# Kernel tuning notes

Measured on AMD Instinct MI355X. Metric: run time of the kernel, lower is better.

The kernel has to match this reference:

```python
import jax, jax.numpy as jnp
import numpy as np

B, S, H, NH = 32, 512, 768, 12
EC, EU = 4, 4
CAP = 1.0
DH = H // NH
CAPACITY = int(CAP * B / EC)  # Switch-style capacity per common expert


def setup_inputs() -> dict:
    key = jax.random.key(0)
    ks = jax.random.split(key, 10)
    s = 0.02
    E = EC + EU  # experts stacked: [0:EC]=common, [EC:]=unique
    return {
        "hidden_states": jax.random.normal(ks[0], (B, S, H), jnp.float32),
        "attention_mask": jnp.zeros((B, S), jnp.float32),  # additive mask
        "Wq": jax.random.normal(ks[1], (E, H, H), jnp.float32) * s,
        "bq": jnp.zeros((E, H), jnp.float32),
        "Wk": jax.random.normal(ks[2], (E, H, H), jnp.float32) * s,
        "bk": jnp.zeros((E, H), jnp.float32),
        "Wv": jax.random.normal(ks[3], (E, H, H), jnp.float32) * s,
        "bv": jnp.zeros((E, H), jnp.float32),
        "Wo": jax.random.normal(ks[4], (E, H, H), jnp.float32) * s,
        "bo": jnp.zeros((E, H), jnp.float32),
        "Wsc": jax.random.normal(ks[5], (H, EC), jnp.float32) * s,
        "bsc": jnp.zeros((EC,), jnp.float32),
        "Wsu": jax.random.normal(ks[6], (H, EU), jnp.float32) * s,
        "bsu": jnp.zeros((EU,), jnp.float32),
    }


def reference(hidden_states, attention_mask, Wq, bq, Wk, bk, Wv, bv, Wo, bo,
              Wsc, bsc, Wsu, bsu):
    # ---- common routing (per-sequence top-1 over mean-pooled tokens) ----
    h_mean = hidden_states.mean(axis=1)                       # [B,H]
    pc = jax.nn.softmax(h_mean @ Wsc + bsc, axis=-1)          # [B,EC]
    rc = jnp.argmax(pc, axis=-1)                              # [B]
    pc_max = jnp.max(pc, axis=-1)                             # [B]
    # capacity drop: within each expert keep the CAPACITY highest-prob seqs
    order = jnp.argsort(-pc_max)                              # global desc sort
    oh = jax.nn.one_hot(rc[order], EC, dtype=jnp.int32)       # [B,EC]
    rank = jnp.take_along_axis(jnp.cumsum(oh, axis=0), rc[order][:, None], 1)[:, 0]
    kept = jnp.zeros((B,), bool).at[order].set(rank <= CAPACITY)

    # ---- unique routing for dropped sequences (mean is per-sequence, so
    #      computing on the full batch and masking matches torch) ----
    pu = jax.nn.softmax(h_mean @ Wsu + bsu, axis=-1)          # [B,EU]
    ru = jnp.argmax(pu, axis=-1)
    pu_max = jnp.max(pu, axis=-1)

    # per-sequence expert index into stacked [EC+EU] expert params
    eidx = jnp.where(kept, rc, EC + ru)                       # [B]
    # scaling factor p/stop_grad(p): ==1 in fwd, routes grads to the gate
    scale = jnp.where(kept,
                      pc_max / jax.lax.stop_gradient(pc_max),
                      pu_max / jax.lax.stop_gradient(pu_max))

    # ---- gather-dispatch: per-sequence expert weights ----
    Wq_b, Wk_b, Wv_b, Wo_b = Wq[eidx], Wk[eidx], Wv[eidx], Wo[eidx]  # [B,H,H]
    bq_b, bk_b, bv_b, bo_b = bq[eidx], bk[eidx], bv[eidx], bo[eidx]  # [B,H]

    def heads(t):  # [B,S,H] -> [B,NH,S,DH]
        return t.reshape(B, S, NH, DH).transpose(0, 2, 1, 3)

    q = heads(jnp.einsum('bsh,bhd->bsd', hidden_states, Wq_b) + bq_b[:, None, :])
    k = heads(jnp.einsum('bsh,bhd->bsd', hidden_states, Wk_b) + bk_b[:, None, :])
    v = heads(jnp.einsum('bsh,bhd->bsd', hidden_states, Wv_b) + bv_b[:, None, :])

    scores = jnp.einsum('bhsd,bhtd->bhst', q, k) / np.float32(np.sqrt(DH))
    scores = scores + attention_mask[:, None, None, :]        # additive mask
    attn = jax.nn.softmax(scores, axis=-1)
    ctx = jnp.einsum('bhst,bhtd->bhsd', attn, v)
    ctx = ctx.transpose(0, 2, 1, 3).reshape(B, S, H)

    out = jnp.einsum('bsh,bhd->bsd', ctx, Wo_b) + bo_b[:, None, :]
    return out * scale[:, None, None]
```

## Files before the change

### kernel.cpp

```cpp
#include <hip/hip_runtime.h>
#include <hip/hip_bf16.h>

#define B_ 32
#define S_ 512
#define H_ 768
#define NH_ 12
#define DH_ 64
#define EC_ 4
#define CAPN_ 8

using short8  = __attribute__((ext_vector_type(8))) short;
using floatx4 = __attribute__((ext_vector_type(4))) float;
using uint2v  = __attribute__((ext_vector_type(2))) unsigned;
using bf16 = __hip_bfloat16;

#define VMCNT(n) asm volatile("s_waitcnt vmcnt(" #n ")" ::: "memory")

__device__ __forceinline__ void gl_lds16(const void* g, void* l) {
  __builtin_amdgcn_global_load_lds(
      (const __attribute__((address_space(1))) unsigned int*)g,
      (__attribute__((address_space(3))) unsigned int*)l, 16, 0, 0);
}

__device__ __forceinline__ unsigned pk2(float lo, float hi) {
  __hip_bfloat162 h = __float22bfloat162_rn(make_float2(lo, hi));
  unsigned r;
  __builtin_memcpy(&r, &h, 4);
  return r;
}

__global__ void k_mean_convert(const float* __restrict__ X, bf16* __restrict__ Xh,
                               float* __restrict__ partial) {
  int idx = blockIdx.x * 256 + threadIdx.x;
  int b = idx / H_, h = idx - b * H_;
  int s0 = blockIdx.y * 64;
  size_t base = ((size_t)b * S_ + s0) * H_ + h;
  float sum = 0.f;
#pragma unroll 8
  for (int s = 0; s < 64; ++s) {
    float v = X[base + (size_t)s * H_];
    Xh[base + (size_t)s * H_] = __float2bfloat16(v);
    sum += v;
  }
  partial[(size_t)blockIdx.y * (B_ * H_) + idx] = sum;
}

__global__ void k_mean_reduce(const float* __restrict__ partial, float* __restrict__ hmean) {
  int idx = blockIdx.x * 256 + threadIdx.x;
  float s = 0.f;
#pragma unroll
  for (int c = 0; c < 8; ++c) s += partial[(size_t)c * (B_ * H_) + idx];
  hmean[idx] = s * (1.f / 512.f);
}

__global__ void k_wt(const float* __restrict__ Wq, const float* __restrict__ Wk,
                     const float* __restrict__ Wv, const float* __restrict__ Wo,
                     bf16* __restrict__ Wt) {
  __shared__ float tile[32][33];
  int z = blockIdx.z;
  const float* Wbase = (z < 8 ? Wq : z < 16 ? Wk : z < 24 ? Wv : Wo) + (size_t)(z & 7) * H_ * H_;
  int k0 = blockIdx.x * 32, n0 = blockIdx.y * 32;
  int tj = threadIdx.x & 31, ti = threadIdx.x >> 5;
#pragma unroll
  for (int r = 0; r < 4; ++r)
    tile[ti + r * 8][tj] = Wbase[(size_t)(k0 + ti + r * 8) * H_ + n0 + tj];
  __syncthreads();
  bf16* out = Wt + (size_t)z * H_ * H_;
#pragma unroll
  for (int r = 0; r < 4; ++r)
    out[(size_t)(n0 + ti + r * 8) * H_ + k0 + tj] = __float2bfloat16(tile[tj][ti + r * 8]);
}

__global__ void k_gate(const float* __restrict__ hmean,
                       const float* __restrict__ Wsc, const float* __restrict__ bsc,
                       const float* __restrict__ Wsu, const float* __restrict__ bsu,
                       float* __restrict__ logits) {
  int b = blockIdx.x;
  int t = threadIdx.x;
  int g = t >> 3, p = t & 7;
  const float* hm = hmean + (size_t)b * H_;
  const float* w;
  float bias;
  if (g < 4) { w = Wsc + g; bias = bsc[g]; }
  else       { w = Wsu + (g - 4); bias = bsu[g - 4]; }
  float acc = 0.f;
  for (int j = p; j < H_; j += 8) acc += hm[j] * w[j * 4];
  acc += __shfl_xor(acc, 1);
  acc += __shfl_xor(acc, 2);
  acc += __shfl_xor(acc, 4);
  if (p == 0) logits[b * 8 + g] = acc + bias;
}

__global__ void k_route2(const float* __restrict__ logits, int* __restrict__ eidx) {
  __shared__ float pcmax[B_];
  __shared__ int rc_s[B_], ru_s[B_];
  int t = threadIdx.x;
  if (t < B_) {
    float lg[8];
#pragma unroll
    for (int e = 0; e < 8; ++e) lg[e] = logits[t * 8 + e];
    float m = lg[0]; int a = 0;
    for (int e = 1; e < 4; ++e) if (lg[e] > m) { m = lg[e]; a = e; }
    float s = 0.f;
    for (int e = 0; e < 4; ++e) s += expf(lg[e] - m);
    pcmax[t] = 1.f / s;
    rc_s[t] = a;
    float mu = lg[4]; int au = 0;
    for (int e = 1; e < 4; ++e) if (lg[4 + e] > mu) { mu = lg[4 + e]; au = e; }
    ru_s[t] = au;
  }
  __syncthreads();
  if (t == 0) {
    bool used[B_], kept[B_];
    int cnt[EC_] = {0, 0, 0, 0};
    for (int i = 0; i < B_; ++i) used[i] = false;
    for (int i = 0; i < B_; ++i) {
      int best = 0; float bv = -1e30f;
      for (int j = 0; j < B_; ++j)
        if (!used[j] && pcmax[j] > bv) { bv = pcmax[j]; best = j; }
      used[best] = true;
      kept[best] = (++cnt[rc_s[best]] <= CAPN_);
    }
    for (int i = 0; i < B_; ++i)
      eidx[i] = kept[i] ? rc_s[i] : EC_ + ru_s[i];
  }
}

template <int OMODE, int NM>
__global__ __launch_bounds__(256, 3) void k_gemm(
    const bf16* __restrict__ A, const bf16* __restrict__ Wt,
    const float* __restrict__ bias0, const float* __restrict__ bias1,
    const float* __restrict__ bias2,
    void* out0, void* out1, void* out2,
    const int* __restrict__ eidx, int mat0) {
  __shared__ __align__(16) char lds[3][16384];
  const int nwg = 96 * NM * 8;
  int wg = blockIdx.x;
  int f = (wg & 7) * (nwg >> 3) + (wg >> 3);
  int b = f / (24 * NM);
  int r0 = f - b * 24 * NM;
  int mat = r0 / 24;
  int tile = r0 - mat * 24;
  int m0 = (tile & 3) * 128, n0 = (tile >> 2) * 128;
  int e = eidx[b];
  const bf16* Ab = A + (size_t)b * S_ * H_;
  const bf16* Wb = Wt + (size_t)((mat0 + mat) * 8 + e) * H_ * H_;
  const float* bias = ((mat == 0) ? bias0 : (mat == 1) ? bias1 : bias2) + (size_t)e * H_;
  void* outp = (mat == 0) ? out0 : (mat == 1) ? out1 : out2;

  int t = threadIdx.x, lane = t & 63, w = t >> 6;
  int wm = (w & 1) * 64, wn = (w >> 1) * 64;
  int lm = lane & 15, lq = lane >> 4;

  auto stage = [&](char* buf, int kt) {
#pragma unroll
    for (int r = 0; r < 4; ++r) {
      int c = t + r * 256;
      int isB = c >> 9;
      int cc = c & 511;
      int row = cc >> 2, pos = cc & 3;
      int kc = pos ^ (row & 3);
      const bf16* g = (isB ? Wb + (size_t)(n0 + row) * H_
                           : Ab + (size_t)(m0 + row) * H_) + kt * 32 + kc * 8;
      gl_lds16(g, buf + (size_t)c * 16);
    }
  };

  floatx4 acc[4][4] = {};
  stage(lds[0], 0);
  stage(lds[1], 1);
  VMCNT(4);
  __builtin_amdgcn_s_barrier();
  __builtin_amdgcn_sched_barrier(0);

  int cb = 0;
  for (int kt = 0; kt < 24; ++kt) {
    if (kt < 22) {
      int pb = cb + 2; if (pb >= 3) pb -= 3;
      stage(lds[pb], kt + 2);
    }
    const char* cur = lds[cb];
    short8 af[4], bfr[4];
#pragma unroll
    for (int mf = 0; mf < 4; ++mf) {
      int mm = wm + mf * 16 + lm;
      af[mf] = *(const short8*)(cur + mm * 64 + ((lq ^ (mm & 3)) * 16));
    }
#pragma unroll
    for (int nf = 0; nf < 4; ++nf) {
      int nn = wn + nf * 16 + lm;
      bfr[nf] = *(const short8*)(cur + 8192 + nn * 64 + ((lq ^ (nn & 3)) * 16));
    }
#pragma unroll
    for (int mf = 0; mf < 4; ++mf)
#pragma unroll
      for (int nf = 0; nf < 4; ++nf)
        acc[mf][nf] = __builtin_amdgcn_mfma_f32_16x16x32_bf16(af[mf], bfr[nf], acc[mf][nf], 0, 0, 0);
    if (kt < 23) {
      if (kt < 22) { VMCNT(4); } else { VMCNT(0); }
      __builtin_amdgcn_s_barrier();
      __builtin_amdgcn_sched_barrier(0);
    }
    ++cb; if (cb == 3) cb = 0;
  }

#pragma unroll
  for (int mf = 0; mf < 4; ++mf) {
#pragma unroll
    for (int nf = 0; nf < 4; ++nf) {
      int n = n0 + wn + nf * 16 + lm;
      float bv = bias[n];
      int mrow = m0 + wm + mf * 16 + lq * 4;
      size_t rowbase = ((size_t)b * S_ + mrow) * H_ + n;
#pragma unroll
      for (int r = 0; r < 4; ++r) {
        float v = acc[mf][nf][r] + bv;
        if (OMODE == 0) {
          if (mat == 2) {
            int s = mrow + r;
            ((bf16*)outp)[((size_t)(b * NH_ + (n >> 6))) * 32768 +
                          (size_t)(s >> 3) * 512 + (n & 63) * 8 + (s & 7)] =
                __float2bfloat16(v);
          } else {
            ((bf16*)outp)[rowbase + (size_t)r * H_] = __float2bfloat16(v);
          }
        } else {
          ((float*)outp)[rowbase + (size_t)r * H_] = v;
        }
      }
    }
  }
}

__global__ __launch_bounds__(256, 3) void k_attn(
    const bf16* __restrict__ Q, const bf16* __restrict__ K,
    const bf16* __restrict__ Vt, const float* __restrict__ mask,
    bf16* __restrict__ Ctx) {
  int bh = blockIdx.x;
  int b = bh / NH_, h = bh - b * NH_;
  int t = threadIdx.x, lane = t & 63, w = t >> 6;
  int lm = lane & 15, lq = lane >> 4;
  int q0 = blockIdx.y * 128 + w * 32;

  short8 qf[2][2];
#pragma unroll
  for (int mf = 0; mf < 2; ++mf)
#pragma unroll
    for (int kf = 0; kf < 2; ++kf)
      qf[mf][kf] = *(const short8*)(Q + ((size_t)(b * S_ + q0 + mf * 16 + lm)) * H_ +
                                    h * DH_ + kf * 32 + lq * 8);

  int kr = ((lm >> 2) << 3) + (lm & 3);
  const int koff[4] = {0, 4, 32, 36};
  const bf16* kbase = K + ((size_t)(b * S_) + kr) * H_ + h * DH_ + lq * 8;
  const bf16* vtb = Vt + ((size_t)(b * NH_ + h)) * 32768;
  const float* mbase = mask + (size_t)b * S_ + lq * 8;

  floatx4 oacc[2][4] = {};
  float m_[2] = {-1e30f, -1e30f}, l_[2] = {0.f, 0.f};

  for (int kt = 0; kt < 8; ++kt) {
    floatx4 sT[2][4] = {};
#pragma unroll
    for (int kf = 0; kf < 2; ++kf) {
      short8 kb4[4];
#pragma unroll
      for (int nf = 0; nf < 4; ++nf)
        kb4[nf] = *(const short8*)(kbase + (size_t)(kt * 64 + koff[nf]) * H_ + kf * 32);
#pragma unroll
      for (int mf = 0; mf < 2; ++mf)
#pragma unroll
        for (int nf = 0; nf < 4; ++nf)
          sT[mf][nf] = __builtin_amdgcn_mfma_f32_16x16x32_bf16(kb4[nf], qf[mf][kf], sT[mf][nf], 0, 0, 0);
    }
    short8 vf[2][4];
#pragma unroll
    for (int kf = 0; kf < 2; ++kf)
#pragma unroll
      for (int nf = 0; nf < 4; ++nf)
        vf[kf][nf] = *(const short8*)(vtb + (size_t)(kt * 8 + kf * 4 + lq) * 512 +
                                      (nf * 16 + lm) * 8);
    const floatx4* mp = (const floatx4*)(mbase + kt * 64);
    floatx4 mv[4] = {mp[0], mp[1], mp[8], mp[9]};

    short8 pf[2][2];
#pragma unroll
    for (int mf = 0; mf < 2; ++mf) {
      float p[4][4];
#pragma unroll
      for (int nf = 0; nf < 4; ++nf)
#pragma unroll
        for (int r = 0; r < 4; ++r)
          p[nf][r] = sT[mf][nf][r] * 0.125f + mv[nf][r];
      float t01 = fmaxf(fmaxf(fmaxf(p[0][0], p[0][1]), fmaxf(p[0][2], p[0][3])),
                        fmaxf(fmaxf(p[1][0], p[1][1]), fmaxf(p[1][2], p[1][3])));
      float t23 = fmaxf(fmaxf(fmaxf(p[2][0], p[2][1]), fmaxf(p[2][2], p[2][3])),
                        fmaxf(fmaxf(p[3][0], p[3][1]), fmaxf(p[3][2], p[3][3])));
      float tm = fmaxf(t01, t23);
      tm = fmaxf(tm, __shfl_xor(tm, 16));
      tm = fmaxf(tm, __shfl_xor(tm, 32));
      float mn = fmaxf(m_[mf], tm);
      float a = __expf(m_[mf] - mn);
      m_[mf] = mn;
      float ps = 0.f;
#pragma unroll
      for (int nf = 0; nf < 4; ++nf)
#pragma unroll
        for (int r = 0; r < 4; ++r) {
          p[nf][r] = __expf(p[nf][r] - mn);
          ps += p[nf][r];
        }
      ps += __shfl_xor(ps, 16);
      ps += __shfl_xor(ps, 32);
      l_[mf] = l_[mf] * a + ps;
#pragma unroll
      for (int nf = 0; nf < 4; ++nf) oacc[mf][nf] *= a;
      union { short8 s8; unsigned u[4]; } pku;
      pku.u[0] = pk2(p[0][0], p[0][1]); pku.u[1] = pk2(p[0][2], p[0][3]);
      pku.u[2] = pk2(p[1][0], p[1][1]); pku.u[3] = pk2(p[1][2], p[1][3]);
      pf[mf][0] = pku.s8;
      pku.u[0] = pk2(p[2][0], p[2][1]); pku.u[1] = pk2(p[2][2], p[2][3]);
      pku.u[2] = pk2(p[3][0], p[3][1]); pku.u[3] = pk2(p[3][2], p[3][3]);
      pf[mf][1] = pku.s8;
    }
#pragma unroll
    for (int kf = 0; kf < 2; ++kf)
#pragma unroll
      for (int mf = 0; mf < 2; ++mf)
#pragma unroll
        for (int nf = 0; nf < 4; ++nf)
          oacc[mf][nf] = __builtin_amdgcn_mfma_f32_16x16x32_bf16(vf[kf][nf], pf[mf][kf], oacc[mf][nf], 0, 0, 0);
  }
#pragma unroll
  for (int mf = 0; mf < 2; ++mf) {
    float inv = 1.f / l_[mf];
    bf16* op = Ctx + ((size_t)(b * S_ + q0 + mf * 16 + lm)) * H_ + h * DH_ + lq * 4;
#pragma unroll
    for (int nf = 0; nf < 4; ++nf) {
      uint2v o;
      o.x = pk2(oacc[mf][nf][0] * inv, oacc[mf][nf][1] * inv);
      o.y = pk2(oacc[mf][nf][2] * inv, oacc[mf][nf][3] * inv);
      *(uint2v*)(op + nf * 16) = o;
    }
  }
}

extern "C" void kernel_launch(void* const* d_in, const int* in_sizes, int n_in,
                              void* d_out, int out_size, void* d_ws, size_t ws_size,
                              hipStream_t stream) {
  const float* X    = (const float*)d_in[0];
  const float* mask = (const float*)d_in[1];
  const float* Wq   = (const float*)d_in[2];
  const float* bq   = (const float*)d_in[3];
  const float* Wk   = (const float*)d_in[4];
  const float* bk   = (const float*)d_in[5];
  const float* Wv   = (const float*)d_in[6];
  const float* bv   = (const float*)d_in[7];
  const float* Wo   = (const float*)d_in[8];
  const float* bo   = (const float*)d_in[9];
  const float* Wsc  = (const float*)d_in[10];
  const float* bsc  = (const float*)d_in[11];
  const float* Wsu  = (const float*)d_in[12];
  const float* bsu  = (const float*)d_in[13];

  char* ws = (char*)d_ws;
  int*   eidx    = (int*)ws;
  float* logits  = (float*)(ws + 128);
  float* partial = (float*)(ws + 1280);
  float* hmean   = (float*)(ws + 787712);
  bf16*  Xh      = (bf16*)(ws + 886016);
  bf16*  Wt      = (bf16*)(ws + 26051840);
  bf16*  qb      = (bf16*)(ws + 63800576);
  bf16*  kb      = (bf16*)(ws + 88966400);
  bf16*  Vt      = (bf16*)(ws + 114132224);
  bf16*  ctx     = Xh;

  k_mean_convert<<<dim3(96, 8), 256, 0, stream>>>(X, Xh, partial);
  k_mean_reduce<<<96, 256, 0, stream>>>(partial, hmean);
  k_wt<<<dim3(24, 24, 32), 256, 0, stream>>>(Wq, Wk, Wv, Wo, Wt);
  k_gate<<<B_, 64, 0, stream>>>(hmean, Wsc, bsc, Wsu, bsu, logits);
  k_route2<<<1, 64, 0, stream>>>(logits, eidx);
  k_gemm<0, 3><<<dim3(2304), 256, 0, stream>>>(Xh, Wt, bq, bk, bv,
                                               (void*)qb, (void*)kb, (void*)Vt, eidx, 0);
  k_attn<<<dim3(B_ * NH_, 4), 256, 0, stream>>>(qb, kb, Vt, mask, ctx);
  k_gemm<1, 1><<<dim3(768), 256, 0, stream>>>(ctx, Wt, bo, bo, bo,
                                              d_out, d_out, d_out, eidx, 3);
}
```

Baseline: 454.2 us.

## Merge prep kernels, fuse routing into one block, widen GEMM K-step to 64

Folds the mean/convert and weight-transpose kernels into a single launch, and merges the mean reduce, gate and routing into one 1024-thread block that keeps the per-sequence mean in LDS. The projection GEMM now stages 64-wide K slices with an 8-way XOR swizzle, double-buffering A and triple-buffering B, and halves the loop trip count. This raises LDS use to 80KB per block, so the launch bound drops to 2 blocks per CU. The intent is fewer launches and fewer barriers per K step, at the cost of occupancy and a serial single-block routing stage.

```diff
diff --git a/kernel.cpp b/kernel.cpp
--- a/kernel.cpp
+++ b/kernel.cpp
@@ -29,76 +29,81 @@
   return r;
 }
 
-__global__ void k_mean_convert(const float* __restrict__ X, bf16* __restrict__ Xh,
-                               float* __restrict__ partial) {
-  int idx = blockIdx.x * 256 + threadIdx.x;
-  int b = idx / H_, h = idx - b * H_;
-  int s0 = blockIdx.y * 64;
-  size_t base = ((size_t)b * S_ + s0) * H_ + h;
-  float sum = 0.f;
+__global__ void k_prep(const float* __restrict__ X, bf16* __restrict__ Xh,
+                       float* __restrict__ partial,
+                       const float* __restrict__ Wq, const float* __restrict__ Wk,
+                       const float* __restrict__ Wv, const float* __restrict__ Wo,
+                       bf16* __restrict__ Wt) {
+  __shared__ float tile[32][33];
+  int f = blockIdx.x;
+  if (f < 768) {
+    int bx = f % 96, by = f / 96;
+    int idx = bx * 256 + threadIdx.x;
+    int b = idx / H_, h = idx - b * H_;
+    int s0 = by * 64;
+    size_t base = ((size_t)b * S_ + s0) * H_ + h;
+    float sum = 0.f;
 #pragma unroll 8
-  for (int s = 0; s < 64; ++s) {
-    float v = X[base + (size_t)s * H_];
-    Xh[base + (size_t)s * H_] = __float2bfloat16(v);
-    sum += v;
-  }
-  partial[(size_t)blockIdx.y * (B_ * H_) + idx] = sum;
-}
-
-__global__ void k_mean_reduce(const float* __restrict__ partial, float* __restrict__ hmean) {
-  int idx = blockIdx.x * 256 + threadIdx.x;
-  float s = 0.f;
-#pragma unroll
-  for (int c = 0; c < 8; ++c) s += partial[(size_t)c * (B_ * H_) + idx];
-  hmean[idx] = s * (1.f / 512.f);
-}
-
-__global__ void k_wt(const float* __restrict__ Wq, const float* __restrict__ Wk,
-                     const float* __restrict__ Wv, const float* __restrict__ Wo,
-                     bf16* __restrict__ Wt) {
-  __shared__ float tile[32][33];
-  int z = blockIdx.z;
-  const float* Wbase = (z < 8 ? Wq : z < 16 ? Wk : z < 24 ? Wv : Wo) + (size_t)(z & 7) * H_ * H_;
-  int k0 = blockIdx.x * 32, n0 = blockIdx.y * 32;
-  int tj = threadIdx.x & 31, ti = threadIdx.x >> 5;
-#pragma unroll
-  for (int r = 0; r < 4; ++r)
-    tile[ti + r * 8][tj] = Wbase[(size_t)(k0 + ti + r * 8) * H_ + n0 + tj];
-  __syncthreads();
-  bf16* out = Wt + (size_t)z * H_ * H_;
-#pragma unroll
-  for (int r = 0; r < 4; ++r)
-    out[(size_t)(n0 + ti + r * 8) * H_ + k0 + tj] = __float2bfloat16(tile[tj][ti + r * 8]);
-}
-
-__global__ void k_gate(const float* __restrict__ hmean,
-                       const float* __restrict__ Wsc, const float* __restrict__ bsc,
-                       const float* __restrict__ Wsu, const float* __restrict__ bsu,
-                       float* __restrict__ logits) {
-  int b = blockIdx.x;
-  int t = threadIdx.x;
-  int g = t >> 3, p = t & 7;
-  const float* hm = hmean + (size_t)b * H_;
-  const float* w;
-  float bias;
-  if (g < 4) { w = Wsc + g; bias = bsc[g]; }
-  else       { w = Wsu + (g - 4); bias = bsu[g - 4]; }
-  float acc = 0.f;
-  for (int j = p; j < H_; j += 8) acc += hm[j] * w[j * 4];
-  acc += __shfl_xor(acc, 1);
-  acc += __shfl_xor(acc, 2);
-  acc += __shfl_xor(acc, 4);
-  if (p == 0) logits[b * 8 + g] = acc + bias;
-}
-
-__global__ void k_route2(const float* __restrict__ logits, int* __restrict__ eidx) {
+    for (int s = 0; s < 64; ++s) {
+      float v = X[base + (size_t)s * H_];
+      Xh[base + (size_t)s * H_] = __float2bfloat16(v);
+      sum += v;
+    }
+    partial[(size_t)by * (B_ * H_) + idx] = sum;
+  } else {
+    int wid = f - 768;
+    int z = wid / 576;
+    int rem = wid - z * 576;
+    int xx = rem / 24, yy = rem - xx * 24;
+    const float* Wbase = (z < 8 ? Wq : z < 16 ? Wk : z < 24 ? Wv : Wo) + (size_t)(z & 7) * H_ * H_;
+    int k0 = xx * 32, n0 = yy * 32;
+    int tj = threadIdx.x & 31, ti = threadIdx.x >> 5;
+#pragma unroll
+    for (int r = 0; r < 4; ++r)
+      tile[ti + r * 8][tj] = Wbase[(size_t)(k0 + ti + r * 8) * H_ + n0 + tj];
+    __syncthreads();
+    bf16* out = Wt + (size_t)z * H_ * H_;
+#pragma unroll
+    for (int r = 0; r < 4; ++r)
+      out[(size_t)(n0 + ti + r * 8) * H_ + k0 + tj] = __float2bfloat16(tile[tj][ti + r * 8]);
+  }
+}
+
+__global__ __launch_bounds__(1024) void k_route_all(
+    const float* __restrict__ partial,
+    const float* __restrict__ Wsc, const float* __restrict__ bsc,
+    const float* __restrict__ Wsu, const float* __restrict__ bsu,
+    int* __restrict__ eidx) {
+  __shared__ float hm[B_ * H_];
+  __shared__ float lg_s[B_ * 8];
   __shared__ float pcmax[B_];
   __shared__ int rc_s[B_], ru_s[B_];
   int t = threadIdx.x;
+  for (int i = t; i < B_ * H_; i += 1024) {
+    float s = 0.f;
+#pragma unroll
+    for (int c = 0; c < 8; ++c) s += partial[(size_t)c * (B_ * H_) + i];
+    hm[i] = s * (1.f / 512.f);
+  }
+  __syncthreads();
+  {
+    int g = t >> 2, p = t & 3;
+    int b = g >> 3, gi = g & 7;
+    const float* w;
+    float bias;
+    if (gi < 4) { w = Wsc + gi; bias = bsc[gi]; }
+    else        { w = Wsu + (gi - 4); bias = bsu[gi - 4]; }
+    float acc = 0.f;
+    for (int j = p; j < H_; j += 4) acc += hm[b * H_ + j] * w[j * 4];
+    acc += __shfl_xor(acc, 1);
+    acc += __shfl_xor(acc, 2);
+    if (p == 0) lg_s[g] = acc + bias;
+  }
+  __syncthreads();
   if (t < B_) {
     float lg[8];
 #pragma unroll
-    for (int e = 0; e < 8; ++e) lg[e] = logits[t * 8 + e];
+    for (int e = 0; e < 8; ++e) lg[e] = lg_s[t * 8 + e];
     float m = lg[0]; int a = 0;
     for (int e = 1; e < 4; ++e) if (lg[e] > m) { m = lg[e]; a = e; }
     float s = 0.f;
@@ -127,13 +132,14 @@
 }
 
 template <int OMODE, int NM>
-__global__ __launch_bounds__(256, 3) void k_gemm(
+__global__ __launch_bounds__(256, 2) void k_gemm(
     const bf16* __restrict__ A, const bf16* __restrict__ Wt,
     const float* __restrict__ bias0, const float* __restrict__ bias1,
     const float* __restrict__ bias2,
     void* out0, void* out1, void* out2,
     const int* __restrict__ eidx, int mat0) {
-  __shared__ __align__(16) char lds[3][16384];
+  __shared__ __align__(16) char ldsA[2][16384];
+  __shared__ __align__(16) char ldsB[3][16384];
   const int nwg = 96 * NM * 8;
   int wg = blockIdx.x;
   int f = (wg & 7) * (nwg >> 3) + (wg >> 3);
@@ -152,56 +158,66 @@
   int wm = (w & 1) * 64, wn = (w >> 1) * 64;
   int lm = lane & 15, lq = lane >> 4;
 
-  auto stage = [&](char* buf, int kt) {
+  auto stageA = [&](char* buf, int kt) {
 #pragma unroll
     for (int r = 0; r < 4; ++r) {
       int c = t + r * 256;
-      int isB = c >> 9;
-      int cc = c & 511;
-      int row = cc >> 2, pos = cc & 3;
-      int kc = pos ^ (row & 3);
-      const bf16* g = (isB ? Wb + (size_t)(n0 + row) * H_
-                           : Ab + (size_t)(m0 + row) * H_) + kt * 32 + kc * 8;
-      gl_lds16(g, buf + (size_t)c * 16);
+      int mm = c >> 3, pos = c & 7;
+      int kc = pos ^ (mm & 7);
+      gl_lds16(Ab + (size_t)(m0 + mm) * H_ + kt * 64 + kc * 8, buf + (size_t)c * 16);
     }
   };
+  auto stageB = [&](char* buf, int kt) {
+#pragma unroll
+    for (int r = 0; r < 4; ++r) {
+      int c = t + r * 256;
+      int nn = c >> 3, pos = c & 7;
+      int kc = pos ^ (nn & 7);
+      gl_lds16(Wb + (size_t)(n0 + nn) * H_ + kt * 64 + kc * 8, buf + (size_t)c * 16);
+    }
+  };
 
   floatx4 acc[4][4] = {};
-  stage(lds[0], 0);
-  stage(lds[1], 1);
+  stageA(ldsA[0], 0);
+  stageB(ldsB[0], 0);
+  stageB(ldsB[1], 1);
   VMCNT(4);
   __builtin_amdgcn_s_barrier();
   __builtin_amdgcn_sched_barrier(0);
 
-  int cb = 0;
-  for (int kt = 0; kt < 24; ++kt) {
-    if (kt < 22) {
-      int pb = cb + 2; if (pb >= 3) pb -= 3;
-      stage(lds[pb], kt + 2);
-    }
-    const char* cur = lds[cb];
-    short8 af[4], bfr[4];
-#pragma unroll
-    for (int mf = 0; mf < 4; ++mf) {
-      int mm = wm + mf * 16 + lm;
-      af[mf] = *(const short8*)(cur + mm * 64 + ((lq ^ (mm & 3)) * 16));
-    }
-#pragma unroll
-    for (int nf = 0; nf < 4; ++nf) {
-      int nn = wn + nf * 16 + lm;
-      bfr[nf] = *(const short8*)(cur + 8192 + nn * 64 + ((lq ^ (nn & 3)) * 16));
-    }
-#pragma unroll
-    for (int mf = 0; mf < 4; ++mf)
-#pragma unroll
-      for (int nf = 0; nf < 4; ++nf)
-        acc[mf][nf] = __builtin_amdgcn_mfma_f32_16x16x32_bf16(af[mf], bfr[nf], acc[mf][nf], 0, 0, 0);
-    if (kt < 23) {
-      if (kt < 22) { VMCNT(4); } else { VMCNT(0); }
+  int bcur = 0, bstage = 2;
+  for (int kt = 0; kt < 12; ++kt) {
+    if (kt < 11) stageA(ldsA[(kt + 1) & 1], kt + 1);
+    if (kt < 10) stageB(ldsB[bstage], kt + 2);
+    const char* curA = ldsA[kt & 1];
+    const char* curB = ldsB[bcur];
+#pragma unroll
+    for (int kf = 0; kf < 2; ++kf) {
+      int kc = kf * 4 + lq;
+      short8 af[4], bfr[4];
+#pragma unroll
+      for (int mf = 0; mf < 4; ++mf) {
+        int mm = wm + mf * 16 + lm;
+        af[mf] = *(const short8*)(curA + ((size_t)(mm * 8 + (kc ^ (mm & 7)))) * 16);
+      }
+#pragma unroll
+      for (int nf = 0; nf < 4; ++nf) {
+        int nn = wn + nf * 16 + lm;
+        bfr[nf] = *(const short8*)(curB + ((size_t)(nn * 8 + (kc ^ (nn & 7)))) * 16);
+      }
+#pragma unroll
+      for (int mf = 0; mf < 4; ++mf)
+#pragma unroll
+        for (int nf = 0; nf < 4; ++nf)
+          acc[mf][nf] = __builtin_amdgcn_mfma_f32_16x16x32_bf16(af[mf], bfr[nf], acc[mf][nf], 0, 0, 0);
+    }
+    if (kt < 11) {
+      if (kt < 10) { VMCNT(4); } else { VMCNT(0); }
       __builtin_amdgcn_s_barrier();
       __builtin_amdgcn_sched_barrier(0);
     }
-    ++cb; if (cb == 3) cb = 0;
+    ++bcur; if (bcur == 3) bcur = 0;
+    ++bstage; if (bstage == 3) bstage = 0;
   }
 
 #pragma unroll
@@ -365,9 +381,7 @@
 
   char* ws = (char*)d_ws;
   int*   eidx    = (int*)ws;
-  float* logits  = (float*)(ws + 128);
   float* partial = (float*)(ws + 1280);
-  float* hmean   = (float*)(ws + 787712);
   bf16*  Xh      = (bf16*)(ws + 886016);
   bf16*  Wt      = (bf16*)(ws + 26051840);
   bf16*  qb      = (bf16*)(ws + 63800576);
@@ -375,11 +389,8 @@
   bf16*  Vt      = (bf16*)(ws + 114132224);
   bf16*  ctx     = Xh;
 
-  k_mean_convert<<<dim3(96, 8), 256, 0, stream>>>(X, Xh, partial);
-  k_mean_reduce<<<96, 256, 0, stream>>>(partial, hmean);
-  k_wt<<<dim3(24, 24, 32), 256, 0, stream>>>(Wq, Wk, Wv, Wo, Wt);
-  k_gate<<<B_, 64, 0, stream>>>(hmean, Wsc, bsc, Wsu, bsu, logits);
-  k_route2<<<1, 64, 0, stream>>>(logits, eidx);
+  k_prep<<<dim3(19200), 256, 0, stream>>>(X, Xh, partial, Wq, Wk, Wv, Wo, Wt);
+  k_route_all<<<dim3(1), 1024, 0, stream>>>(partial, Wsc, bsc, Wsu, bsu, eidx);
   k_gemm<0, 3><<<dim3(2304), 256, 0, stream>>>(Xh, Wt, bq, bk, bv,
                                                (void*)qb, (void*)kb, (void*)Vt, eidx, 0);
   k_attn<<<dim3(B_ * NH_, 4), 256, 0, stream>>>(qb, kb, Vt, mask, ctx);
```

Result: slower. 586.1 us (+29.0%).
